# Kernel tuning notes

Measured on AMD Instinct MI355X. Metric: run time of the kernel, lower is better.

The kernel has to match this reference:

```python
import jax, jax.numpy as jnp
import numpy as np

NG, N, NFG, NFR, NFP, B = 4, 64, 1024, 256, 256, 2048
SCALE = 1.0 / float(np.sqrt(NFR + NFP))
EPS = 1e-5  # torch LayerNorm default


def setup_inputs() -> dict:
    key = jax.random.key(0)
    k = jax.random.split(key, 4)
    x = jax.random.normal(k[0], (B, N, NFG), dtype=jnp.float32)
    # per-graph params stacked over NG for vectorized computation
    Wt = jax.random.normal(k[1], (NG, NFR, NFG), dtype=jnp.float32) * 0.02
    bt = jnp.zeros((NG, NFR), dtype=jnp.float32)
    Wp = jax.random.normal(k[2], (NG, NFR, NFG), dtype=jnp.float32) * 0.02
    bp = jnp.zeros((NG, NFR), dtype=jnp.float32)
    Wg = jax.random.normal(k[3], (NG, NFG, NFG), dtype=jnp.float32) * 0.02  # [out,in]
    gamma = jnp.ones((NG, NFG), dtype=jnp.float32)
    beta = jnp.zeros((NG, NFG), dtype=jnp.float32)
    return {"x": x, "Wt": Wt, "bt": bt, "Wp": Wp, "bp": bp,
            "Wg": Wg, "gamma": gamma, "beta": beta}


def reference(x, Wt, bt, Wp, bp, Wg, gamma, beta):
    # theta/phi projections, vectorized over NG graphs: [G,B,N,R]
    theta = jnp.einsum('bnf,grf->gbnr', x, Wt) + bt[:, None, None, :]
    phi = jnp.einsum('bnf,grf->gbnr', x, Wp) + bp[:, None, None, :]
    # original computes sim=theta@phi^T then .sum(2); identical math:
    # relation[b,n] = theta[b,n] . sum_m phi[b,m]  (avoids the NxN matrix)
    phi_sum = phi.sum(axis=2)                                  # [G,B,R]
    relation = jnp.einsum('gbnr,gbr->gbn', theta, phi_sum) * SCALE
    w = jax.nn.softmax(relation, axis=2)                       # softmax over boxes N
    # attention-weighted aggregation over boxes -> [G,B,NFG]
    agg = jnp.einsum('gbn,bnf->gbf', w, x)
    # GCN linear (no bias): [G,B,NFG]
    h = jnp.einsum('gbf,gof->gbo', agg, Wg)
    # LayerNorm over feature dim, per graph
    mu = h.mean(axis=-1, keepdims=True)
    var = ((h - mu) ** 2).mean(axis=-1, keepdims=True)
    h = (h - mu) * jax.lax.rsqrt(var + EPS) * gamma[:, None, :] + beta[:, None, :]
    h = jax.nn.relu(h)
    # mean over the NG graphs; restore keepdim axis -> [B,1,NFG]
    return h.mean(axis=0)[:, None, :]
```

## Files before the change

### kernel.cpp

```cpp
#include <hip/hip_runtime.h>
#include <hip/hip_bf16.h>

typedef __attribute__((ext_vector_type(4))) float f4;
typedef __attribute__((ext_vector_type(4))) float f32x4;
typedef __attribute__((ext_vector_type(8))) short short8;
typedef __attribute__((ext_vector_type(2))) unsigned int u32x2;
typedef __attribute__((ext_vector_type(4))) unsigned int u32x4;
typedef unsigned int u32;
typedef unsigned short u16;

#define SCALE_F 0.04419417382415922f

__device__ inline u16 f2bf(float f) {
  u32 u = __float_as_uint(f);
  u32 r = u + 0x7FFFu + ((u >> 16) & 1u);
  return (u16)(r >> 16);
}
__device__ inline float bflo(u32 u) { return __uint_as_float(u << 16); }
__device__ inline float bfhi(u32 u) { return __uint_as_float(u & 0xFFFF0000u); }

#define GLD16(gsrc, ldst)                                                     \
  __builtin_amdgcn_global_load_lds(                                           \
      (const __attribute__((address_space(1))) void*)(gsrc),                  \
      (__attribute__((address_space(3))) void*)(ldst), 16, 0, 0)

__global__ __launch_bounds__(256) void k0_cvt(const float* __restrict__ src,
                                              u16* __restrict__ dst) {
  int i = blockIdx.x * 256 + threadIdx.x;
  const f4* s = (const f4*)src;
  f4 a = s[(size_t)i * 2];
  f4 b = s[(size_t)i * 2 + 1];
  u32x4 p;
  p[0] = (u32)f2bf(a[0]) | ((u32)f2bf(a[1]) << 16);
  p[1] = (u32)f2bf(a[2]) | ((u32)f2bf(a[3]) << 16);
  p[2] = (u32)f2bf(b[0]) | ((u32)f2bf(b[1]) << 16);
  p[3] = (u32)f2bf(b[2]) | ((u32)f2bf(b[3]) << 16);
  *(u32x4*)(dst + (size_t)i * 8) = p;
}

__global__ __launch_bounds__(256) void k0_wt(const float* __restrict__ Wt,
                                             u16* __restrict__ Wtt) {
  const int g = blockIdx.z;
  const int f0 = blockIdx.x * 64, r0 = blockIdx.y * 64;
  __shared__ u16 tile[64][66];
  const int t = threadIdx.x;
  const float* src = Wt + ((size_t)g * 256 + r0) * 1024 + f0;
#pragma unroll
  for (int i = 0; i < 16; ++i) {
    int idx = t + i * 256;
    int rl = idx >> 6, fl = idx & 63;
    tile[fl][rl] = f2bf(src[rl * 1024 + fl]);
  }
  __syncthreads();
  u16* dst = Wtt + ((size_t)g * 1024 + f0) * 256 + r0;
#pragma unroll
  for (int i = 0; i < 4; ++i) {
    int idx = t + i * 256;
    int fl = idx >> 4, rq = idx & 15;
    u32x2 p;
    p[0] = (u32)tile[fl][rq * 4]     | ((u32)tile[fl][rq * 4 + 1] << 16);
    p[1] = (u32)tile[fl][rq * 4 + 2] | ((u32)tile[fl][rq * 4 + 3] << 16);
    *(u32x2*)(dst + fl * 256 + rq * 4) = p;
  }
}

__global__ __launch_bounds__(256) void k1_colsum(const float* __restrict__ x,
                                                 u16* __restrict__ xs16) {
  int b = blockIdx.x, t = threadIdx.x;
  const float* xb = x + (size_t)b * (64 * 1024);
  f4 acc = {0.f, 0.f, 0.f, 0.f};
#pragma unroll 8
  for (int n = 0; n < 64; ++n)
    acc += *(const f4*)(xb + n * 1024 + t * 4);
  u32x2 p;
  p[0] = (u32)f2bf(acc[0]) | ((u32)f2bf(acc[1]) << 16);
  p[1] = (u32)f2bf(acc[2]) | ((u32)f2bf(acc[3]) << 16);
  *(u32x2*)(xs16 + (size_t)b * 1024 + t * 4) = p;
}

__global__ __launch_bounds__(256) void k2_gemm(const u16* __restrict__ A,
                                               const u16* __restrict__ Bt,
                                               const float* __restrict__ bp,
                                               u16* __restrict__ C) {
  const int n0 = blockIdx.x * 128, m0 = blockIdx.y * 128;
  __shared__ u16 Al[128 * 32];
  __shared__ u16 Bl[128 * 32];
  const int t = threadIdx.x;
  const int w = t >> 6, l = t & 63;
  const int wr = w >> 1, wc = w & 1;
  const int lr = l & 15, lh = l >> 4;
  f32x4 acc[4][4] = {};
  for (int kt = 0; kt < 1024; kt += 32) {
#pragma unroll
    for (int j = 0; j < 2; ++j) {
      int idx = t + j * 256;
      int row = idx >> 2, sl = idx & 3;
      GLD16(A + (size_t)(m0 + row) * 1024 + kt + sl * 8, Al + idx * 8);
      GLD16(Bt + (size_t)(n0 + row) * 1024 + kt + sl * 8, Bl + idx * 8);
    }
    __syncthreads();
    short8 af[4], bfr[4];
#pragma unroll
    for (int m = 0; m < 4; ++m)
      af[m] = *(const short8*)(Al + (wr * 64 + m * 16 + lr) * 32 + lh * 8);
#pragma unroll
    for (int n = 0; n < 4; ++n)
      bfr[n] = *(const short8*)(Bl + (wc * 64 + n * 16 + lr) * 32 + lh * 8);
#pragma unroll
    for (int m = 0; m < 4; ++m)
#pragma unroll
      for (int n = 0; n < 4; ++n)
        acc[m][n] = __builtin_amdgcn_mfma_f32_16x16x32_bf16(af[m], bfr[n],
                                                            acc[m][n], 0, 0, 0);
    __syncthreads();
  }
#pragma unroll
  for (int m = 0; m < 4; ++m)
#pragma unroll
    for (int n = 0; n < 4; ++n) {
      int col = n0 + wc * 64 + n * 16 + lr;
      float bb = 64.0f * bp[col];
#pragma unroll
      for (int j = 0; j < 4; ++j)
        C[(size_t)(m0 + wr * 64 + m * 16 + lh * 4 + j) * 1024 + col] =
            f2bf(acc[m][n][j] + bb);
    }
}

__global__ __launch_bounds__(256) void k3_gemm(const u16* __restrict__ A,
                                               const u16* __restrict__ Btt,
                                               float* __restrict__ V) {
  const int g = blockIdx.z;
  const int n0 = blockIdx.x * 128, m0 = blockIdx.y * 128;
  const u16* Bg = Btt + (size_t)g * 1024 * 256;
  __shared__ u16 Al[128 * 32];
  __shared__ u16 Bl[128 * 32];
  const int t = threadIdx.x;
  const int w = t >> 6, l = t & 63;
  const int wr = w >> 1, wc = w & 1;
  const int lr = l & 15, lh = l >> 4;
  f32x4 acc[4][4] = {};
  for (int kt = 0; kt < 256; kt += 32) {
#pragma unroll
    for (int j = 0; j < 2; ++j) {
      int idx = t + j * 256;
      int row = idx >> 2, sl = idx & 3;
      GLD16(A + (size_t)(m0 + row) * 1024 + g * 256 + kt + sl * 8, Al + idx * 8);
      GLD16(Bg + (size_t)(n0 + row) * 256 + kt + sl * 8, Bl + idx * 8);
    }
    __syncthreads();
    short8 af[4], bfr[4];
#pragma unroll
    for (int m = 0; m < 4; ++m)
      af[m] = *(const short8*)(Al + (wr * 64 + m * 16 + lr) * 32 + lh * 8);
#pragma unroll
    for (int n = 0; n < 4; ++n)
      bfr[n] = *(const short8*)(Bl + (wc * 64 + n * 16 + lr) * 32 + lh * 8);
#pragma unroll
    for (int m = 0; m < 4; ++m)
#pragma unroll
      for (int n = 0; n < 4; ++n)
        acc[m][n] = __builtin_amdgcn_mfma_f32_16x16x32_bf16(af[m], bfr[n],
                                                            acc[m][n], 0, 0, 0);
    __syncthreads();
  }
  float* Vg = V + (size_t)g * 2048 * 1024;
#pragma unroll
  for (int m = 0; m < 4; ++m)
#pragma unroll
    for (int n = 0; n < 4; ++n)
#pragma unroll
      for (int j = 0; j < 4; ++j)
        Vg[(size_t)(m0 + wr * 64 + m * 16 + lh * 4 + j) * 1024 +
           (n0 + wc * 64 + n * 16 + lr)] = acc[m][n][j];
}

#define K4_LDS (131072 + 8256 + 16384 + 1024)
__global__ __launch_bounds__(1024) void k4_fused(const float* __restrict__ x,
                                                 const float* __restrict__ V,
                                                 u16* __restrict__ aggb) {
  extern __shared__ char sm[];
  char* xl = sm;
  u16* vb = (u16*)(sm + 131072);
  float* relp = (float*)(sm + 139328);
  float* wsm = (float*)(sm + 155712);
  const int t = threadIdx.x;
  const int b = blockIdx.x;
  const float* xb = x + (size_t)b * 65536;

  f4 xr[8];
#pragma unroll
  for (int i = 0; i < 8; ++i) {
    int u = i * 1024 + t;
    xr[i] = *(const f4*)(xb + (u >> 7) * 1024 + (u & 127) * 4);
  }
  f4 va = *(const f4*)(V + ((size_t)(t >> 8) * 2048 + b) * 1024 + (t & 255) * 4);
#pragma unroll
  for (int i = 0; i < 8; ++i) {
    int u = i * 1024 + t;
    int row = u >> 7, col4 = u & 127;
    u32 p0 = (u32)f2bf(xr[i][0]) | ((u32)f2bf(xr[i][1]) << 16);
    u32 p1 = (u32)f2bf(xr[i][2]) | ((u32)f2bf(xr[i][3]) << 16);
    int slot = col4 >> 1, half = col4 & 1;
    char* dst = xl + row * 2048 + ((slot ^ (row & 7)) << 4) + half * 8;
    ((u32*)dst)[0] = p0;
    ((u32*)dst)[1] = p1;
  }
  {
    int g = t >> 8, q = t & 255;
    u32x2 p;
    p[0] = (u32)f2bf(va[0]) | ((u32)f2bf(va[1]) << 16);
    p[1] = (u32)f2bf(va[2]) | ((u32)f2bf(va[3]) << 16);
    *(u32x2*)(vb + g * 1032 + q * 4) = p;
  }
  f4 xr2[8];
#pragma unroll
  for (int i = 0; i < 8; ++i) {
    int u = i * 1024 + t;
    xr2[i] = *(const f4*)(xb + (u >> 7) * 1024 + (u & 127) * 4 + 512);
  }
  asm volatile("s_waitcnt lgkmcnt(0)" ::: "memory");
  __builtin_amdgcn_s_barrier();

  const int w = t >> 6, l = t & 63, lg = l >> 4, lr = l & 15;
  f32x4 racc[4] = {};
  {
    const int kt = w * 32;
    short8 afr = {};
    if (lr < 4)
      afr = *(const short8*)(vb + lr * 1032 + kt + lg * 8);
#pragma unroll
    for (int nt = 0; nt < 4; ++nt) {
      int n = nt * 16 + lr;
      short8 bfrg = *(const short8*)(
          xl + n * 2048 + ((((kt >> 3) + lg) ^ (n & 7)) << 4));
      racc[nt] = __builtin_amdgcn_mfma_f32_16x16x32_bf16(afr, bfrg, racc[nt],
                                                         0, 0, 0);
    }
  }
#pragma unroll
  for (int i = 0; i < 8; ++i) {
    int u = i * 1024 + t;
    int row = u >> 7, col4 = 128 + (u & 127);
    u32 p0 = (u32)f2bf(xr2[i][0]) | ((u32)f2bf(xr2[i][1]) << 16);
    u32 p1 = (u32)f2bf(xr2[i][2]) | ((u32)f2bf(xr2[i][3]) << 16);
    int slot = col4 >> 1, half = col4 & 1;
    char* dst = xl + row * 2048 + ((slot ^ (row & 7)) << 4) + half * 8;
    ((u32*)dst)[0] = p0;
    ((u32*)dst)[1] = p1;
  }
  asm volatile("s_waitcnt lgkmcnt(0)" ::: "memory");
  __builtin_amdgcn_s_barrier();

  {
    const int kt = 512 + w * 32;
    short8 afr = {};
    if (lr < 4)
      afr = *(const short8*)(vb + lr * 1032 + kt + lg * 8);
#pragma unroll
    for (int nt = 0; nt < 4; ++nt) {
      int n = nt * 16 + lr;
      short8 bfrg = *(const short8*)(
          xl + n * 2048 + ((((kt >> 3) + lg) ^ (n & 7)) << 4));
      racc[nt] = __builtin_amdgcn_mfma_f32_16x16x32_bf16(afr, bfrg, racc[nt],
                                                         0, 0, 0);
    }
  }
  if (l < 16) {
#pragma unroll
    for (int nt = 0; nt < 4; ++nt)
#pragma unroll
      for (int j = 0; j < 4; ++j)
        relp[(w * 4 + j) * 64 + nt * 16 + lr] = racc[nt][j];
  }
  __syncthreads();

  if (t < 256) {
    const int g = t >> 6, n = t & 63;
    float rel = 0.f;
#pragma unroll
    for (int ww = 0; ww < 16; ++ww) rel += relp[(ww * 4 + g) * 64 + n];
    rel *= SCALE_F;
    float mx = rel;
#pragma unroll
    for (int o = 32; o > 0; o >>= 1) mx = fmaxf(mx, __shfl_xor(mx, o, 64));
    float e = __expf(rel - mx);
    float s = e;
#pragma unroll
    for (int o = 32; o > 0; o >>= 1) s += __shfl_xor(s, o, 64);
    wsm[t] = e / s;
  }
  __syncthreads();

  {
    const int hh = t >> 9, r = t & 511, g = r >> 7, f8 = r & 127;
    const float* wg = wsm + g * 64 + hh * 32;
    float a0 = 0, a1 = 0, a2 = 0, a3 = 0, a4 = 0, a5 = 0, a6 = 0, a7 = 0;
#pragma unroll 8
    for (int n0 = 0; n0 < 32; ++n0) {
      int n = hh * 32 + n0;
      float wv = wg[n0];
      u32x4 xp = *(const u32x4*)(xl + n * 2048 + ((f8 ^ (n & 7)) << 4));
      a0 = fmaf(bflo(xp[0]), wv, a0);
      a1 = fmaf(bfhi(xp[0]), wv, a1);
      a2 = fmaf(bflo(xp[1]), wv, a2);
      a3 = fmaf(bfhi(xp[1]), wv, a3);
      a4 = fmaf(bflo(xp[2]), wv, a4);
      a5 = fmaf(bfhi(xp[2]), wv, a5);
      a6 = fmaf(bflo(xp[3]), wv, a6);
      a7 = fmaf(bfhi(xp[3]), wv, a7);
    }
    if (hh) {
      f4 q0 = {a0, a1, a2, a3};
      f4 q1 = {a4, a5, a6, a7};
      *(f4*)(relp + r * 8) = q0;
      *(f4*)(relp + r * 8 + 4) = q1;
    }
    __syncthreads();
    if (!hh) {
      f4 q0 = *(const f4*)(relp + r * 8);
      f4 q1 = *(const f4*)(relp + r * 8 + 4);
      u32x4 p;
      p[0] = (u32)f2bf(a0 + q0[0]) | ((u32)f2bf(a1 + q0[1]) << 16);
      p[1] = (u32)f2bf(a2 + q0[2]) | ((u32)f2bf(a3 + q0[3]) << 16);
      p[2] = (u32)f2bf(a4 + q1[0]) | ((u32)f2bf(a5 + q1[1]) << 16);
      p[3] = (u32)f2bf(a6 + q1[2]) | ((u32)f2bf(a7 + q1[3]) << 16);
      *(u32x4*)(aggb + ((size_t)g * 2048 + b) * 1024 + f8 * 8) = p;
    }
  }
}

__global__ __launch_bounds__(256) void k5_gemm(const u16* __restrict__ Ab,
                                               const u16* __restrict__ Bb,
                                               float* __restrict__ H) {
  const int g = blockIdx.z;
  const int n0 = blockIdx.x * 128, m0 = blockIdx.y * 128;
  const u16* A = Ab + (size_t)g * 2048 * 1024;
  const u16* Bt = Bb + (size_t)g * 1024 * 1024;
  __shared__ u16 Al[128 * 32];
  __shared__ u16 Bl[128 * 32];
  const int t = threadIdx.x;
  const int w = t >> 6, l = t & 63;
  const int wr = w >> 1, wc = w & 1;
  const int lr = l & 15, lh = l >> 4;
  f32x4 acc[4][4] = {};
  for (int kt = 0; kt < 1024; kt += 32) {
#pragma unroll
    for (int j = 0; j < 2; ++j) {
      int idx = t + j * 256;
      int row = idx >> 2, sl = idx & 3;
      GLD16(A + (size_t)(m0 + row) * 1024 + kt + sl * 8, Al + idx * 8);
      GLD16(Bt + (size_t)(n0 + row) * 1024 + kt + sl * 8, Bl + idx * 8);
    }
    __syncthreads();
    short8 af[4], bfr[4];
#pragma unroll
    for (int m = 0; m < 4; ++m)
      af[m] = *(const short8*)(Al + (wr * 64 + m * 16 + lr) * 32 + lh * 8);
#pragma unroll
    for (int n = 0; n < 4; ++n)
      bfr[n] = *(const short8*)(Bl + (wc * 64 + n * 16 + lr) * 32 + lh * 8);
#pragma unroll
    for (int m = 0; m < 4; ++m)
#pragma unroll
      for (int n = 0; n < 4; ++n)
        acc[m][n] = __builtin_amdgcn_mfma_f32_16x16x32_bf16(af[m], bfr[n],
                                                            acc[m][n], 0, 0, 0);
    __syncthreads();
  }
  float* Hg = H + (size_t)g * 2048 * 1024;
#pragma unroll
  for (int m = 0; m < 4; ++m)
#pragma unroll
    for (int n = 0; n < 4; ++n)
#pragma unroll
      for (int j = 0; j < 4; ++j)
        Hg[(size_t)(m0 + wr * 64 + m * 16 + lh * 4 + j) * 1024 +
           (n0 + wc * 64 + n * 16 + lr)] = acc[m][n][j];
}

__global__ __launch_bounds__(256) void k6_ln(const float* __restrict__ H,
                                             const float* __restrict__ gamma,
                                             const float* __restrict__ beta,
                                             float* __restrict__ out) {
  const int b = blockIdx.x, t = threadIdx.x;
  const int w = t >> 6, lane = t & 63;
  __shared__ float red[8];
  f4 acc = {0.f, 0.f, 0.f, 0.f};
  for (int g = 0; g < 4; ++g) {
    f4 hv = *(const f4*)(H + ((size_t)g * 2048 + b) * 1024 + t * 4);
    float s = hv[0] + hv[1] + hv[2] + hv[3];
    float q = hv[0] * hv[0] + hv[1] * hv[1] + hv[2] * hv[2] + hv[3] * hv[3];
#pragma unroll
    for (int o = 32; o > 0; o >>= 1) {
      s += __shfl_xor(s, o, 64);
      q += __shfl_xor(q, o, 64);
    }
    if (lane == 0) { red[w] = s; red[4 + w] = q; }
    __syncthreads();
    s = red[0] + red[1] + red[2] + red[3];
    q = red[4] + red[5] + red[6] + red[7];
    float mean = s * (1.f / 1024.f);
    float var = q * (1.f / 1024.f) - mean * mean;
    float rstd = rsqrtf(var + 1e-5f);
    f4 gm = *(const f4*)(gamma + g * 1024 + t * 4);
    f4 bt = *(const f4*)(beta + g * 1024 + t * 4);
#pragma unroll
    for (int j = 0; j < 4; ++j) {
      float val = (hv[j] - mean) * rstd * gm[j] + bt[j];
      acc[j] += fmaxf(val, 0.f);
    }
    __syncthreads();
  }
  acc *= 0.25f;
  *(f4*)(out + (size_t)b * 1024 + t * 4) = acc;
}

extern "C" void kernel_launch(void* const* d_in, const int* in_sizes, int n_in,
                              void* d_out, int out_size, void* d_ws, size_t ws_size,
                              hipStream_t stream) {
  const float* x     = (const float*)d_in[0];
  const float* Wt    = (const float*)d_in[1];
  const float* Wp    = (const float*)d_in[3];
  const float* bp    = (const float*)d_in[4];
  const float* Wg    = (const float*)d_in[5];
  const float* gamma = (const float*)d_in[6];
  const float* beta  = (const float*)d_in[7];
  float* out = (float*)d_out;

  char* ws = (char*)d_ws;
  u16*   xs16 = (u16*)(ws);
  u16*   ps16 = (u16*)(ws + (4u << 20));
  u16*   wpb  = (u16*)(ws + (8u << 20));
  u16*   wtb  = (u16*)(ws + (10u << 20));
  u16*   wgb  = (u16*)(ws + (12u << 20));
  float* v    = (float*)(ws + (20u << 20));
  float* h    = (float*)(ws + (20u << 20));
  u16*   aggb = (u16*)(ws + (52u << 20));

  hipFuncSetAttribute((const void*)k4_fused,
                      hipFuncAttributeMaxDynamicSharedMemorySize, K4_LDS);

  k0_cvt<<<2048, 256, 0, stream>>>(Wg, wgb);
  k0_cvt<<<512, 256, 0, stream>>>(Wp, wpb);
  k0_wt<<<dim3(16, 4, 4), 256, 0, stream>>>(Wt, wtb);
  k1_colsum<<<2048, 256, 0, stream>>>(x, xs16);
  k2_gemm<<<dim3(8, 16), 256, 0, stream>>>(xs16, wpb, bp, ps16);
  k3_gemm<<<dim3(8, 16, 4), 256, 0, stream>>>(ps16, wtb, v);
  k4_fused<<<2048, 1024, K4_LDS, stream>>>(x, v, aggb);
  k5_gemm<<<dim3(8, 16, 4), 256, 0, stream>>>(aggb, wgb, h);
  k6_ln<<<2048, 256, 0, stream>>>(h, gamma, beta, out);
}
```

Before: 349.7 us.

## Pre-swizzle bf16 x in colsum pass, bf16 intermediates, two batches per fused block

```diff
diff --git a/kernel.cpp b/kernel.cpp
--- a/kernel.cpp
+++ b/kernel.cpp
@@ -64,14 +64,24 @@
   }
 }
 
-__global__ __launch_bounds__(256) void k1_colsum(const float* __restrict__ x,
-                                                 u16* __restrict__ xs16) {
-  int b = blockIdx.x, t = threadIdx.x;
-  const float* xb = x + (size_t)b * (64 * 1024);
+__global__ __launch_bounds__(256) void k1_prep(const float* __restrict__ x,
+                                               u16* __restrict__ xs16,
+                                               char* __restrict__ xpre) {
+  const int b = blockIdx.x, t = threadIdx.x;
+  const float* xb = x + (size_t)b * 65536;
+  char* xp = xpre + (size_t)b * 131072;
+  const int slot = t >> 1, half = t & 1;
   f4 acc = {0.f, 0.f, 0.f, 0.f};
 #pragma unroll 8
-  for (int n = 0; n < 64; ++n)
-    acc += *(const f4*)(xb + n * 1024 + t * 4);
+  for (int n = 0; n < 64; ++n) {
+    f4 v = *(const f4*)(xb + n * 1024 + t * 4);
+    acc += v;
+    u32 p0 = (u32)f2bf(v[0]) | ((u32)f2bf(v[1]) << 16);
+    u32 p1 = (u32)f2bf(v[2]) | ((u32)f2bf(v[3]) << 16);
+    char* dst = xp + n * 2048 + ((slot ^ (n & 7)) << 4) + half * 8;
+    ((u32*)dst)[0] = p0;
+    ((u32*)dst)[1] = p1;
+  }
   u32x2 p;
   p[0] = (u32)f2bf(acc[0]) | ((u32)f2bf(acc[1]) << 16);
   p[1] = (u32)f2bf(acc[2]) | ((u32)f2bf(acc[3]) << 16);
@@ -129,7 +139,7 @@
 
 __global__ __launch_bounds__(256) void k3_gemm(const u16* __restrict__ A,
                                                const u16* __restrict__ Btt,
-                                               float* __restrict__ V) {
+                                               u16* __restrict__ Vb) {
   const int g = blockIdx.z;
   const int n0 = blockIdx.x * 128, m0 = blockIdx.y * 128;
   const u16* Bg = Btt + (size_t)g * 1024 * 256;
@@ -164,7 +174,7 @@
                                                             acc[m][n], 0, 0, 0);
     __syncthreads();
   }
-  float* Vg = V + (size_t)g * 2048 * 1024;
+  u16* Vg = Vb + (size_t)g * 2048 * 1024;
 #pragma unroll
   for (int m = 0; m < 4; ++m)
 #pragma unroll
@@ -172,63 +182,18 @@
 #pragma unroll
       for (int j = 0; j < 4; ++j)
         Vg[(size_t)(m0 + wr * 64 + m * 16 + lh * 4 + j) * 1024 +
-           (n0 + wc * 64 + n * 16 + lr)] = acc[m][n][j];
-}
-
-#define K4_LDS (131072 + 8256 + 16384 + 1024)
-__global__ __launch_bounds__(1024) void k4_fused(const float* __restrict__ x,
-                                                 const float* __restrict__ V,
-                                                 u16* __restrict__ aggb) {
-  extern __shared__ char sm[];
-  char* xl = sm;
-  u16* vb = (u16*)(sm + 131072);
-  float* relp = (float*)(sm + 139328);
-  float* wsm = (float*)(sm + 155712);
-  const int t = threadIdx.x;
-  const int b = blockIdx.x;
-  const float* xb = x + (size_t)b * 65536;
-
-  f4 xr[8];
-#pragma unroll
-  for (int i = 0; i < 8; ++i) {
-    int u = i * 1024 + t;
-    xr[i] = *(const f4*)(xb + (u >> 7) * 1024 + (u & 127) * 4);
-  }
-  f4 va = *(const f4*)(V + ((size_t)(t >> 8) * 2048 + b) * 1024 + (t & 255) * 4);
-#pragma unroll
-  for (int i = 0; i < 8; ++i) {
-    int u = i * 1024 + t;
-    int row = u >> 7, col4 = u & 127;
-    u32 p0 = (u32)f2bf(xr[i][0]) | ((u32)f2bf(xr[i][1]) << 16);
-    u32 p1 = (u32)f2bf(xr[i][2]) | ((u32)f2bf(xr[i][3]) << 16);
-    int slot = col4 >> 1, half = col4 & 1;
-    char* dst = xl + row * 2048 + ((slot ^ (row & 7)) << 4) + half * 8;
-    ((u32*)dst)[0] = p0;
-    ((u32*)dst)[1] = p1;
-  }
-  {
-    int g = t >> 8, q = t & 255;
-    u32x2 p;
-    p[0] = (u32)f2bf(va[0]) | ((u32)f2bf(va[1]) << 16);
-    p[1] = (u32)f2bf(va[2]) | ((u32)f2bf(va[3]) << 16);
-    *(u32x2*)(vb + g * 1032 + q * 4) = p;
-  }
-  f4 xr2[8];
-#pragma unroll
-  for (int i = 0; i < 8; ++i) {
-    int u = i * 1024 + t;
-    xr2[i] = *(const f4*)(xb + (u >> 7) * 1024 + (u & 127) * 4 + 512);
-  }
-  asm volatile("s_waitcnt lgkmcnt(0)" ::: "memory");
-  __builtin_amdgcn_s_barrier();
-
-  const int w = t >> 6, l = t & 63, lg = l >> 4, lr = l & 15;
+           (n0 + wc * 64 + n * 16 + lr)] = f2bf(acc[m][n][j]);
+}
+
+__device__ __forceinline__ void relation_phase(const char* xl, const u16* vb,
+                                               float* relp, int w, int l) {
+  const int lg = l >> 4, lr = l & 15;
   f32x4 racc[4] = {};
-  {
-    const int kt = w * 32;
+#pragma unroll
+  for (int kp = 0; kp < 2; ++kp) {
+    const int kt = kp * 512 + w * 32;
     short8 afr = {};
-    if (lr < 4)
-      afr = *(const short8*)(vb + lr * 1032 + kt + lg * 8);
+    if (lr < 4) afr = *(const short8*)(vb + lr * 1032 + kt + lg * 8);
 #pragma unroll
     for (int nt = 0; nt < 4; ++nt) {
       int n = nt * 16 + lr;
@@ -238,34 +203,6 @@
                                                          0, 0, 0);
     }
   }
-#pragma unroll
-  for (int i = 0; i < 8; ++i) {
-    int u = i * 1024 + t;
-    int row = u >> 7, col4 = 128 + (u & 127);
-    u32 p0 = (u32)f2bf(xr2[i][0]) | ((u32)f2bf(xr2[i][1]) << 16);
-    u32 p1 = (u32)f2bf(xr2[i][2]) | ((u32)f2bf(xr2[i][3]) << 16);
-    int slot = col4 >> 1, half = col4 & 1;
-    char* dst = xl + row * 2048 + ((slot ^ (row & 7)) << 4) + half * 8;
-    ((u32*)dst)[0] = p0;
-    ((u32*)dst)[1] = p1;
-  }
-  asm volatile("s_waitcnt lgkmcnt(0)" ::: "memory");
-  __builtin_amdgcn_s_barrier();
-
-  {
-    const int kt = 512 + w * 32;
-    short8 afr = {};
-    if (lr < 4)
-      afr = *(const short8*)(vb + lr * 1032 + kt + lg * 8);
-#pragma unroll
-    for (int nt = 0; nt < 4; ++nt) {
-      int n = nt * 16 + lr;
-      short8 bfrg = *(const short8*)(
-          xl + n * 2048 + ((((kt >> 3) + lg) ^ (n & 7)) << 4));
-      racc[nt] = __builtin_amdgcn_mfma_f32_16x16x32_bf16(afr, bfrg, racc[nt],
-                                                         0, 0, 0);
-    }
-  }
   if (l < 16) {
 #pragma unroll
     for (int nt = 0; nt < 4; ++nt)
@@ -273,8 +210,10 @@
       for (int j = 0; j < 4; ++j)
         relp[(w * 4 + j) * 64 + nt * 16 + lr] = racc[nt][j];
   }
-  __syncthreads();
-
+}
+
+__device__ __forceinline__ void softmax_phase(const float* relp, float* wsm,
+                                              int t) {
   if (t < 256) {
     const int g = t >> 6, n = t & 63;
     float rel = 0.f;
@@ -290,49 +229,114 @@
     for (int o = 32; o > 0; o >>= 1) s += __shfl_xor(s, o, 64);
     wsm[t] = e / s;
   }
-  __syncthreads();
+}
+
+__device__ __forceinline__ void agg_phase(const char* xl, const float* wsm,
+                                          float* relp, u16* aggb, int b,
+                                          int t) {
+  const int hh = t >> 9, r = t & 511, g = r >> 7, f8 = r & 127;
+  const float* wg = wsm + g * 64 + hh * 32;
+  float a0 = 0, a1 = 0, a2 = 0, a3 = 0, a4 = 0, a5 = 0, a6 = 0, a7 = 0;
+#pragma unroll 8
+  for (int n0 = 0; n0 < 32; ++n0) {
+    int n = hh * 32 + n0;
+    float wv = wg[n0];
+    u32x4 xp = *(const u32x4*)(xl + n * 2048 + ((f8 ^ (n & 7)) << 4));
+    a0 = fmaf(bflo(xp[0]), wv, a0);
+    a1 = fmaf(bfhi(xp[0]), wv, a1);
+    a2 = fmaf(bflo(xp[1]), wv, a2);
+    a3 = fmaf(bfhi(xp[1]), wv, a3);
+    a4 = fmaf(bflo(xp[2]), wv, a4);
+    a5 = fmaf(bfhi(xp[2]), wv, a5);
+    a6 = fmaf(bflo(xp[3]), wv, a6);
+    a7 = fmaf(bfhi(xp[3]), wv, a7);
+  }
+  if (hh) {
+    f4 q0 = {a0, a1, a2, a3};
+    f4 q1 = {a4, a5, a6, a7};
+    *(f4*)(relp + r * 8) = q0;
+    *(f4*)(relp + r * 8 + 4) = q1;
+  }
+  __syncthreads();
+  if (!hh) {
+    f4 q0 = *(const f4*)(relp + r * 8);
+    f4 q1 = *(const f4*)(relp + r * 8 + 4);
+    u32x4 p;
+    p[0] = (u32)f2bf(a0 + q0[0]) | ((u32)f2bf(a1 + q0[1]) << 16);
+    p[1] = (u32)f2bf(a2 + q0[2]) | ((u32)f2bf(a3 + q0[3]) << 16);
+    p[2] = (u32)f2bf(a4 + q1[0]) | ((u32)f2bf(a5 + q1[1]) << 16);
+    p[3] = (u32)f2bf(a6 + q1[2]) | ((u32)f2bf(a7 + q1[3]) << 16);
+    *(u32x4*)(aggb + ((size_t)g * 2048 + b) * 1024 + f8 * 8) = p;
+  }
+}
+
+#define K4_LDS (131072 + 8256 + 16384 + 1024)
+__global__ __launch_bounds__(1024) void k4_fused(const char* __restrict__ xpre,
+                                                 const u16* __restrict__ vb16,
+                                                 u16* __restrict__ aggb) {
+  extern __shared__ char sm[];
+  char* xl = sm;
+  u16* vb = (u16*)(sm + 131072);
+  float* relp = (float*)(sm + 131072 + 8256);
+  float* wsm = (float*)(sm + 131072 + 8256 + 16384);
+  const int t = threadIdx.x;
+  const int w = t >> 6, l = t & 63;
+  const int b0 = blockIdx.x * 2, b1 = b0 + 1;
 
   {
-    const int hh = t >> 9, r = t & 511, g = r >> 7, f8 = r & 127;
-    const float* wg = wsm + g * 64 + hh * 32;
-    float a0 = 0, a1 = 0, a2 = 0, a3 = 0, a4 = 0, a5 = 0, a6 = 0, a7 = 0;
-#pragma unroll 8
-    for (int n0 = 0; n0 < 32; ++n0) {
-      int n = hh * 32 + n0;
-      float wv = wg[n0];
-      u32x4 xp = *(const u32x4*)(xl + n * 2048 + ((f8 ^ (n & 7)) << 4));
-      a0 = fmaf(bflo(xp[0]), wv, a0);
-      a1 = fmaf(bfhi(xp[0]), wv, a1);
-      a2 = fmaf(bflo(xp[1]), wv, a2);
-      a3 = fmaf(bfhi(xp[1]), wv, a3);
-      a4 = fmaf(bflo(xp[2]), wv, a4);
-      a5 = fmaf(bfhi(xp[2]), wv, a5);
-      a6 = fmaf(bflo(xp[3]), wv, a6);
-      a7 = fmaf(bfhi(xp[3]), wv, a7);
-    }
-    if (hh) {
-      f4 q0 = {a0, a1, a2, a3};
-      f4 q1 = {a4, a5, a6, a7};
-      *(f4*)(relp + r * 8) = q0;
-      *(f4*)(relp + r * 8 + 4) = q1;
-    }
-    __syncthreads();
-    if (!hh) {
-      f4 q0 = *(const f4*)(relp + r * 8);
-      f4 q1 = *(const f4*)(relp + r * 8 + 4);
-      u32x4 p;
-      p[0] = (u32)f2bf(a0 + q0[0]) | ((u32)f2bf(a1 + q0[1]) << 16);
-      p[1] = (u32)f2bf(a2 + q0[2]) | ((u32)f2bf(a3 + q0[3]) << 16);
-      p[2] = (u32)f2bf(a4 + q1[0]) | ((u32)f2bf(a5 + q1[1]) << 16);
-      p[3] = (u32)f2bf(a6 + q1[2]) | ((u32)f2bf(a7 + q1[3]) << 16);
-      *(u32x4*)(aggb + ((size_t)g * 2048 + b) * 1024 + f8 * 8) = p;
-    }
-  }
+    int g = t >> 8, q = t & 255;
+    u32x2 pv = *(const u32x2*)(vb16 + ((size_t)g * 2048 + b0) * 1024 + q * 4);
+    *(u32x2*)(vb + g * 1032 + q * 4) = pv;
+  }
+  const char* xg0 = xpre + (size_t)b0 * 131072;
+#pragma unroll
+  for (int i = 0; i < 8; ++i)
+    GLD16(xg0 + (w * 8 + i) * 1024 + l * 16, xl + (w * 8 + i) * 1024 + l * 16);
+  __syncthreads();
+
+  const char* xg1 = xpre + (size_t)b1 * 131072;
+  u32x4 pf0 = *(const u32x4*)(xg1 + t * 16);
+  u32x4 pf1 = *(const u32x4*)(xg1 + t * 16 + 16384);
+  u32x4 pf2 = *(const u32x4*)(xg1 + t * 16 + 32768);
+  u32x4 pf3 = *(const u32x4*)(xg1 + t * 16 + 49152);
+  u32x4 pf4 = *(const u32x4*)(xg1 + t * 16 + 65536);
+  u32x4 pf5 = *(const u32x4*)(xg1 + t * 16 + 81920);
+  u32x4 pf6 = *(const u32x4*)(xg1 + t * 16 + 98304);
+  u32x4 pf7 = *(const u32x4*)(xg1 + t * 16 + 114688);
+  u32x2 pv1 =
+      *(const u32x2*)(vb16 + ((size_t)(t >> 8) * 2048 + b1) * 1024 + (t & 255) * 4);
+
+  relation_phase(xl, vb, relp, w, l);
+  __syncthreads();
+  softmax_phase(relp, wsm, t);
+  __syncthreads();
+  agg_phase(xl, wsm, relp, aggb, b0, t);
+  __syncthreads();
+
+  *(u32x4*)(xl + t * 16) = pf0;
+  *(u32x4*)(xl + t * 16 + 16384) = pf1;
+  *(u32x4*)(xl + t * 16 + 32768) = pf2;
+  *(u32x4*)(xl + t * 16 + 49152) = pf3;
+  *(u32x4*)(xl + t * 16 + 65536) = pf4;
+  *(u32x4*)(xl + t * 16 + 81920) = pf5;
+  *(u32x4*)(xl + t * 16 + 98304) = pf6;
+  *(u32x4*)(xl + t * 16 + 114688) = pf7;
+  {
+    int g = t >> 8, q = t & 255;
+    *(u32x2*)(vb + g * 1032 + q * 4) = pv1;
+  }
+  __syncthreads();
+
+  relation_phase(xl, vb, relp, w, l);
+  __syncthreads();
+  softmax_phase(relp, wsm, t);
+  __syncthreads();
+  agg_phase(xl, wsm, relp, aggb, b1, t);
 }
 
 __global__ __launch_bounds__(256) void k5_gemm(const u16* __restrict__ Ab,
                                                const u16* __restrict__ Bb,
-                                               float* __restrict__ H) {
+                                               u16* __restrict__ H) {
   const int g = blockIdx.z;
   const int n0 = blockIdx.x * 128, m0 = blockIdx.y * 128;
   const u16* A = Ab + (size_t)g * 2048 * 1024;
@@ -368,7 +372,7 @@
                                                             acc[m][n], 0, 0, 0);
     __syncthreads();
   }
-  float* Hg = H + (size_t)g * 2048 * 1024;
+  u16* Hg = H + (size_t)g * 2048 * 1024;
 #pragma unroll
   for (int m = 0; m < 4; ++m)
 #pragma unroll
@@ -376,10 +380,10 @@
 #pragma unroll
       for (int j = 0; j < 4; ++j)
         Hg[(size_t)(m0 + wr * 64 + m * 16 + lh * 4 + j) * 1024 +
-           (n0 + wc * 64 + n * 16 + lr)] = acc[m][n][j];
-}
-
-__global__ __launch_bounds__(256) void k6_ln(const float* __restrict__ H,
+           (n0 + wc * 64 + n * 16 + lr)] = f2bf(acc[m][n][j]);
+}
+
+__global__ __launch_bounds__(256) void k6_ln(const u16* __restrict__ H,
                                              const float* __restrict__ gamma,
                                              const float* __restrict__ beta,
                                              float* __restrict__ out) {
@@ -388,7 +392,8 @@
   __shared__ float red[8];
   f4 acc = {0.f, 0.f, 0.f, 0.f};
   for (int g = 0; g < 4; ++g) {
-    f4 hv = *(const f4*)(H + ((size_t)g * 2048 + b) * 1024 + t * 4);
+    u32x2 hp = *(const u32x2*)(H + ((size_t)g * 2048 + b) * 1024 + t * 4);
+    f4 hv = {bflo(hp[0]), bfhi(hp[0]), bflo(hp[1]), bfhi(hp[1])};
     float s = hv[0] + hv[1] + hv[2] + hv[3];
     float q = hv[0] * hv[0] + hv[1] * hv[1] + hv[2] * hv[2] + hv[3] * hv[3];
 #pragma unroll
@@ -434,9 +439,10 @@
   u16*   wpb  = (u16*)(ws + (8u << 20));
   u16*   wtb  = (u16*)(ws + (10u << 20));
   u16*   wgb  = (u16*)(ws + (12u << 20));
-  float* v    = (float*)(ws + (20u << 20));
-  float* h    = (float*)(ws + (20u << 20));
-  u16*   aggb = (u16*)(ws + (52u << 20));
+  u16*   vb16 = (u16*)(ws + (20u << 20));
+  u16*   aggb = (u16*)(ws + (36u << 20));
+  u16*   hb16 = (u16*)(ws + (52u << 20));
+  char*  xpre = (char*)(ws + (68u << 20));
 
   hipFuncSetAttribute((const void*)k4_fused,
                       hipFuncAttributeMaxDynamicSharedMemorySize, K4_LDS);
@@ -444,10 +450,10 @@
   k0_cvt<<<2048, 256, 0, stream>>>(Wg, wgb);
   k0_cvt<<<512, 256, 0, stream>>>(Wp, wpb);
   k0_wt<<<dim3(16, 4, 4), 256, 0, stream>>>(Wt, wtb);
-  k1_colsum<<<2048, 256, 0, stream>>>(x, xs16);
+  k1_prep<<<2048, 256, 0, stream>>>(x, xs16, xpre);
   k2_gemm<<<dim3(8, 16), 256, 0, stream>>>(xs16, wpb, bp, ps16);
-  k3_gemm<<<dim3(8, 16, 4), 256, 0, stream>>>(ps16, wtb, v);
-  k4_fused<<<2048, 1024, K4_LDS, stream>>>(x, v, aggb);
-  k5_gemm<<<dim3(8, 16, 4), 256, 0, stream>>>(aggb, wgb, h);
-  k6_ln<<<2048, 256, 0, stream>>>(h, gamma, beta, out);
-}
+  k3_gemm<<<dim3(8, 16, 4), 256, 0, stream>>>(ps16, wtb, vb16);
+  k4_fused<<<1024, 1024, K4_LDS, stream>>>(xpre, vb16, aggb);
+  k5_gemm<<<dim3(8, 16, 4), 256, 0, stream>>>(aggb, wgb, hb16);
+  k6_ln<<<2048, 256, 0, stream>>>(hb16, gamma, beta, out);
+}
```

Measured after the change: 346.6 us. About the same (-0.9%).
